# Optimization experiments

Hardware: AMD Instinct MI355X
Metric: run time of the kernel (lower is better)

## Reference

```python
import jax, jax.numpy as jnp
import numpy as np

L, N, D, T = 24, 576, 4096, 128
RED = D // 4           # DSU reduced dim (reduction_ratio=4)
FOCUS = (-2) % L       # focus layer index = 22
EPS_LN = 1e-5          # torch LayerNorm default eps
EPS_SC = 1e-6          # score-normalization eps
N_FOCUS = 32           # final_focus (hardcoded in forward)
N_NONFOCUS = 32        # final_nonfocus (hardcoded in forward)
MIN_ACTIVE = 8
THRESH = 3.0


def _ln(x, g=None, b=None):
    mu = x.mean(-1, keepdims=True)
    var = ((x - mu) ** 2).mean(-1, keepdims=True)
    y = (x - mu) / jnp.sqrt(var + EPS_LN)
    if g is not None:
        y = y * g + b
    return y


def setup_inputs() -> dict:
    key = jax.random.key(0)
    ks = jax.random.split(key, 10)
    rn = lambda k, shape, s=0.02: jax.random.normal(k, shape, jnp.float32) * s
    z = lambda n: jnp.zeros((n,), jnp.float32)
    return {
        'text_features': jax.random.normal(ks[0], (T, D), jnp.float32),
        'layer_feats': jax.random.normal(ks[1], (L, N, D), jnp.float32),
        'W1': rn(ks[2], (RED, 3 * D)), 'b1': z(RED),
        'Wc': rn(ks[3], (D, RED)), 'bc_lin': z(D), 'bc': z(D),
        'Wi': rn(ks[4], (D, RED)), 'bi_lin': z(D), 'bi': z(D),
        'Wf': rn(ks[5], (D, RED)), 'bf_lin': z(D), 'bf': z(D),
        'score_q_w': rn(ks[6], (D, D)), 'score_k_w': rn(ks[7], (D, D)),
        'ln_g': jnp.ones((D,), jnp.float32), 'ln_b': z(D),
        'layer_logits': rn(ks[8], (L,), 0.1),
        'scale': jnp.array([0.1], jnp.float32),
    }


def reference(text_features, layer_feats, W1, b1, Wc, bc_lin, bc, Wi, bi_lin, bi,
              Wf, bf_lin, bf, score_q_w, score_k_w, ln_g, ln_b, layer_logits, scale):
    # --- text conditioning ---
    text_global = _ln(text_features.mean(0))                 # [D]
    y = layer_feats.mean(1)                                   # [L, D] per-layer pooled

    # --- DSU recurrence over layers (LSTM-like cell) ---
    def dsu(c_prev, y_l):
        comb = jnp.concatenate([jax.nn.sigmoid(c_prev), y_l, text_global])
        s = jax.nn.relu(W1 @ comb + b1)                       # [RED]
        c_t = jnp.tanh(Wc @ s + bc_lin + bc)
        i = jax.nn.sigmoid(Wi @ s + bi_lin + bi)
        f = jax.nn.sigmoid(Wf @ s + bf_lin + bf)
        c = f * c_prev + i * c_t
        return c, c

    _, ctx = jax.lax.scan(dsu, jnp.zeros((D,), text_features.dtype), y)  # [L, D]

    # --- per-layer scores with LayerNorm'd q/k ---
    q = _ln(ctx @ score_q_w.T, ln_g, ln_b)                    # [L, D]
    kf = _ln(layer_feats @ score_k_w.T, ln_g, ln_b)           # [L, N, D]
    raw = jnp.einsum('lnd,ld->ln', kf, q)                     # [L, N]
    mu = raw.mean(1, keepdims=True)
    sd = raw.std(1, keepdims=True) + EPS_SC                   # unbiased=False
    scores = (raw - mu) / sd                                  # [L, N]
    conf = scores.max(1)                                      # [L]

    # --- active-layer selection (threshold path vs top-8 fallback) ---
    nonfocus = jnp.ones((L,), bool).at[FOCUS].set(False)
    conf_nf = jnp.where(nonfocus, conf, -jnp.inf)
    act_t = nonfocus & (conf > THRESH)
    M_t = act_t.sum()
    _, idx_f = jax.lax.top_k(conf_nf, MIN_ACTIVE)             # fallback: top-8 conf, desc
    act_f = jnp.zeros((L,), bool).at[idx_f].set(True)
    pos_f = jnp.full((L,), L, jnp.int32).at[idx_f].set(jnp.arange(MIN_ACTIVE, dtype=jnp.int32))
    pos_t = jnp.cumsum(act_t.astype(jnp.int32)) - 1           # ascending layer order
    use_fb = M_t < MIN_ACTIVE
    act = jnp.where(use_fb, act_f, act_t)
    pos = jnp.where(use_fb, pos_f, pos_t)
    M = jnp.where(use_fb, MIN_ACTIVE, M_t)

    # --- budget split: base per active layer + remainder to earliest (N=576 >> 32, no deficit) ---
    base = N_NONFOCUS // M
    rem = N_NONFOCUS - base * M
    k_nf = jnp.where(act, base + (pos < rem).astype(jnp.int32), 0)  # [L], sums to 32

    # --- per-layer top-32 indices (sorted desc), gather evidence ---
    _, top_idx = jax.lax.top_k(scores, N_FOCUS)               # [L, 32]
    ev_focus = layer_feats[FOCUS][top_idx[FOCUS]]             # [32, D]
    cum = jnp.cumsum(k_nf)                                    # [L]
    t = jnp.arange(N_NONFOCUS)
    li = jnp.searchsorted(cum, t, side='right')               # owning layer per slot
    r = t - (cum[li] - k_nf[li])                              # rank within layer
    ev_nf = layer_feats[li, top_idx[li, r]]                   # [32, D]

    # --- anchor-residual layer mix + 3x3 group pooling ---
    logits = layer_logits.astype(jnp.float32).at[FOCUS].set(-jnp.inf)
    alpha = jax.nn.softmax(logits)                            # [L], alpha[anchor]=0
    anchor = layer_feats[FOCUS]                               # [N, D]
    delta = jnp.einsum('l,lnd->nd', alpha, layer_feats - anchor[None])
    x_mix = anchor + scale[0] * delta                         # [576, D]
    groups = x_mix.reshape(3, 8, 3, 8, D).transpose(0, 2, 1, 3, 4).reshape(9, 64, D).mean(1)

    return jnp.concatenate([ev_focus, ev_nf, groups], 0)      # [73, D]
```

## Files before the change

### kernel.cpp

```cpp
#include <hip/hip_runtime.h>
#include <stdint.h>
#include <math.h>

#define LAY 24
#define NTOK 576
#define DIM 4096
#define TTXT 128
#define REDD 1024
#define FOCUSL 22

typedef unsigned int u32;
typedef unsigned short u16;
typedef float f32x4 __attribute__((ext_vector_type(4)));
typedef short bf16x8 __attribute__((ext_vector_type(8)));
typedef u16 u16x4 __attribute__((ext_vector_type(4)));

__device__ __forceinline__ u16 f2bf(float f) {
  u32 u = __builtin_bit_cast(u32, f);
  u32 r = u + 0x7fffu + ((u >> 16) & 1u);
  return (u16)(r >> 16);
}
__device__ __forceinline__ float sigm(float x) { return 1.0f / (1.0f + expf(-x)); }

#define GLOBAL_AS __attribute__((address_space(1)))
#define LDS_AS __attribute__((address_space(3)))
__device__ __forceinline__ void gld_lds16(const void* g, void* l) {
  __builtin_amdgcn_global_load_lds((const GLOBAL_AS u32*)g, (LDS_AS u32*)l, 16, 0, 0);
}

__global__ void k_text_colmean(const float* __restrict__ tf, float* __restrict__ tmean) {
  int c = blockIdx.x * 256 + threadIdx.x;
  float s = 0.f;
  for (int r = 0; r < TTXT; r++) s += tf[(size_t)r * DIM + c];
  tmean[c] = s * (1.0f / TTXT);
}

__global__ void k_text_ln(const float* __restrict__ tmean, float* __restrict__ tg) {
  __shared__ float red[256];
  int t = threadIdx.x;
  float x[16]; float s = 0.f;
  for (int i = 0; i < 16; i++) { x[i] = tmean[i * 256 + t]; s += x[i]; }
  red[t] = s; __syncthreads();
  for (int o = 128; o; o >>= 1) { if (t < o) red[t] += red[t + o]; __syncthreads(); }
  float mean = red[0] / DIM; __syncthreads();
  float q = 0.f;
  for (int i = 0; i < 16; i++) { float d = x[i] - mean; q += d * d; }
  red[t] = q; __syncthreads();
  for (int o = 128; o; o >>= 1) { if (t < o) red[t] += red[t + o]; __syncthreads(); }
  float var = red[0] / DIM;
  float rinv = 1.0f / sqrtf(var + 1e-5f);
  for (int i = 0; i < 16; i++) tg[i * 256 + t] = (x[i] - mean) * rinv;
}

__global__ void k_pass_a(const float* __restrict__ x, u16* __restrict__ xb,
                         float* __restrict__ gm) {
  int bid = blockIdx.x;
  int a = bid % 3, dc = (bid / 3) & 7, l = bid / 24;
  int d4 = dc * 512 + threadIdx.x * 4;
  f32x4 acc[3] = {};
  int n0 = a * 192;
  const float* p = x + ((size_t)(l * NTOK + n0)) * DIM + d4;
  u16* q = xb + ((size_t)(l * NTOK + n0)) * DIM + d4;
  for (int nn = 0; nn < 192; nn++) {
    f32x4 v = *(const f32x4*)p;
    u16x4 bv; bv.x = f2bf(v.x); bv.y = f2bf(v.y); bv.z = f2bf(v.z); bv.w = f2bf(v.w);
    *(u16x4*)q = bv;
    int c = (nn >> 3) % 3;
    acc[c] += v;
    p += DIM; q += DIM;
  }
  for (int c = 0; c < 3; c++) {
    f32x4 o = acc[c] * (1.0f / 64.0f);
    *(f32x4*)(gm + ((size_t)(l * 9 + a * 3 + c)) * DIM + d4) = o;
  }
}

__global__ void k_y(const float* __restrict__ gm, float* __restrict__ y) {
  int bid = blockIdx.x;
  int l = bid >> 2, dc = bid & 3;
  int d4 = dc * 1024 + threadIdx.x * 4;
  f32x4 s = {};
  for (int g = 0; g < 9; g++) s += *(const f32x4*)(gm + ((size_t)(l * 9 + g)) * DIM + d4);
  *(f32x4*)(y + (size_t)l * DIM + d4) = s * (1.0f / 9.0f);
}

__global__ void k_conv_wk(const float* __restrict__ wk, u16* __restrict__ wkb) {
  size_t i = (size_t)blockIdx.x * 256 + threadIdx.x;
  f32x4 v = ((const f32x4*)wk)[i];
  u16x4 b; b.x = f2bf(v.x); b.y = f2bf(v.y); b.z = f2bf(v.z); b.w = f2bf(v.w);
  ((u16x4*)wkb)[i] = b;
}

__global__ __launch_bounds__(256) void k_gemm_s2(const u16* __restrict__ xb,
                                                 const u16* __restrict__ wkb,
                                                 float* __restrict__ s2p) {
  __shared__ __align__(16) u16 As[128 * 32];
  __shared__ __align__(16) u16 Bs[128 * 32];
  int bid = blockIdx.x;
  int mt = bid >> 5, nt = bid & 31;
  int tid = threadIdx.x;
  int wid = tid >> 6, lane = tid & 63;
  int wm = (wid >> 1) * 64, wn = (wid & 1) * 64;
  int lm = lane & 15, qq = lane >> 4;
  f32x4 acc[4][4] = {};
  const u16* gA = xb + (size_t)(mt * 128) * DIM;
  const u16* gB = wkb + (size_t)(nt * 128) * DIM;
  for (int kt = 0; kt < DIM / 32; kt++) {
    int k0 = kt * 32;
    __syncthreads();
    for (int j = 0; j < 2; j++) {
      int seg = tid + 256 * j;
      int row = seg >> 2, ko = (seg & 3) * 8;
      gld_lds16(gA + (size_t)row * DIM + k0 + ko, &As[seg * 8]);
      gld_lds16(gB + (size_t)row * DIM + k0 + ko, &Bs[seg * 8]);
    }
    __syncthreads();
    bf16x8 aF[4], bF[4];
    for (int mi = 0; mi < 4; mi++) aF[mi] = *(const bf16x8*)&As[(wm + mi * 16 + lm) * 32 + qq * 8];
    for (int ni = 0; ni < 4; ni++) bF[ni] = *(const bf16x8*)&Bs[(wn + ni * 16 + lm) * 32 + qq * 8];
    for (int mi = 0; mi < 4; mi++)
      for (int ni = 0; ni < 4; ni++)
        acc[mi][ni] = __builtin_amdgcn_mfma_f32_16x16x32_bf16(aF[mi], bF[ni], acc[mi][ni], 0, 0, 0);
  }
  for (int mi = 0; mi < 4; mi++) {
    for (int reg = 0; reg < 4; reg++) {
      float s = 0.f;
      for (int ni = 0; ni < 4; ni++) { float v = acc[mi][ni][reg]; s += v * v; }
      for (int off = 1; off < 16; off <<= 1) s += __shfl_xor(s, off, 64);
      if (lm == 0) {
        int row = mt * 128 + wm + mi * 16 + qq * 4 + reg;
        s2p[(size_t)row * 64 + nt * 2 + (wid & 1)] = s;
      }
    }
  }
}

__global__ void k_s2_reduce(const float* __restrict__ s2p, float* __restrict__ S2) {
  int row = blockIdx.x * 256 + threadIdx.x;
  const f32x4* p = (const f32x4*)(s2p + (size_t)row * 64);
  float s = 0.f;
  for (int i = 0; i < 16; i++) { f32x4 v = p[i]; s += v.x + v.y + v.z + v.w; }
  S2[row] = s;
}

__global__ __launch_bounds__(256) void k_pre(const float* __restrict__ W1, const float* __restrict__ b1,
                                             const float* __restrict__ y, const float* __restrict__ tg,
                                             float* __restrict__ pre) {
  int r = blockIdx.x, t = threadIdx.x;
  __shared__ float ylds[LAY][256];
  __shared__ float tglds[256];
  __shared__ float red[256];
  float acc[LAY]; for (int l = 0; l < LAY; l++) acc[l] = 0.f;
  float accc = 0.f;
  const float* wb = W1 + (size_t)r * (3 * DIM) + DIM;
  const float* wc = W1 + (size_t)r * (3 * DIM) + 2 * DIM;
  for (int ch = 0; ch < 16; ch++) {
    for (int l = 0; l < LAY; l++) ylds[l][t] = y[(size_t)l * DIM + ch * 256 + t];
    tglds[t] = tg[ch * 256 + t];
    __syncthreads();
    float w1b = wb[ch * 256 + t];
    float w1c = wc[ch * 256 + t];
    for (int l = 0; l < LAY; l++) acc[l] += w1b * ylds[l][t];
    accc += w1c * tglds[t];
    __syncthreads();
  }
  red[t] = accc; __syncthreads();
  for (int o = 128; o; o >>= 1) { if (t < o) red[t] += red[t + o]; __syncthreads(); }
  float csum = red[0]; __syncthreads();
  for (int l = 0; l < LAY; l++) {
    red[t] = acc[l]; __syncthreads();
    for (int o = 128; o; o >>= 1) { if (t < o) red[t] += red[t + o]; __syncthreads(); }
    if (t == 0) pre[l * REDD + r] = b1[r] + red[0] + csum;
    __syncthreads();
  }
}

__global__ void k_dsu_init(float* __restrict__ c_prev, float* __restrict__ u) {
  int i = blockIdx.x * 256 + threadIdx.x;
  c_prev[i] = 0.0f;
  u[i] = 0.5f;
}

__global__ __launch_bounds__(256) void k_dsu1(const float* __restrict__ W1, const float* __restrict__ pre,
                                              const float* __restrict__ u, float* __restrict__ svec,
                                              int l) {
  __shared__ __align__(16) float ulds[DIM];
  int b = blockIdx.x, t = threadIdx.x;
  int wid = t >> 6, lane = t & 63;
  for (int i = 0; i < 16; i++) ulds[i * 256 + t] = u[i * 256 + t];
  __syncthreads();
  int r = b * 4 + wid;
  const float* wrow = W1 + (size_t)r * (3 * DIM);
  float acc = 0.f;
  for (int i = 0; i < 16; i++) {
    int e = i * 256 + lane * 4;
    f32x4 w = *(const f32x4*)(wrow + e);
    f32x4 uv = *(const f32x4*)(&ulds[e]);
    acc += w.x * uv.x + w.y * uv.y + w.z * uv.z + w.w * uv.w;
  }
  for (int off = 32; off; off >>= 1) acc += __shfl_down(acc, off, 64);
  if (lane == 0) {
    float sv = acc + pre[l * REDD + r];
    svec[r] = sv > 0.f ? sv : 0.f;
  }
}

__global__ __launch_bounds__(256) void k_dsu2(
    const float* __restrict__ Wc, const float* __restrict__ Wi, const float* __restrict__ Wf,
    const float* __restrict__ bc_lin, const float* __restrict__ bc,
    const float* __restrict__ bi_lin, const float* __restrict__ bi,
    const float* __restrict__ bf_lin, const float* __restrict__ bf,
    const float* __restrict__ svec, float* __restrict__ c_prev, float* __restrict__ u,
    float* __restrict__ ctx, int l) {
  __shared__ __align__(16) float sl[REDD];
  int b = blockIdx.x, t = threadIdx.x;
  int wid = t >> 6, lane = t & 63;
  for (int i = 0; i < 4; i++) sl[i * 256 + t] = svec[i * 256 + t];
  __syncthreads();
  int d = b * 4 + wid;
  float g3[3];
  for (int gate = 0; gate < 3; gate++) {
    const float* wrow = (gate == 0 ? Wc : (gate == 1 ? Wi : Wf)) + (size_t)d * REDD;
    float acc = 0.f;
    for (int i = 0; i < 4; i++) {
      int k = i * 256 + lane * 4;
      f32x4 w = *(const f32x4*)(wrow + k);
      f32x4 sv = *(const f32x4*)(&sl[k]);
      acc += w.x * sv.x + w.y * sv.y + w.z * sv.z + w.w * sv.w;
    }
    for (int off = 32; off; off >>= 1) acc += __shfl_down(acc, off, 64);
    g3[gate] = acc;
  }
  if (lane == 0) {
    float ct = tanhf(g3[0] + bc_lin[d] + bc[d]);
    float iv = sigm(g3[1] + bi_lin[d] + bi[d]);
    float fv = sigm(g3[2] + bf_lin[d] + bf[d]);
    float c = fv * c_prev[d] + iv * ct;
    c_prev[d] = c;
    u[d] = sigm(c);
    ctx[(size_t)l * DIM + d] = c;
  }
}

__global__ __launch_bounds__(256) void k_qpre(const float* __restrict__ ctx, const float* __restrict__ Wq,
                                              float* __restrict__ qpre) {
  __shared__ __align__(16) float clds[LAY][512];
  int b = blockIdx.x, t = threadIdx.x;
  int wid = t >> 6, lane = t & 63;
  int e = b * 4 + wid;
  const float* wrow = Wq + (size_t)e * DIM;
  float acc[LAY]; for (int l = 0; l < LAY; l++) acc[l] = 0.f;
  for (int ch = 0; ch < 8; ch++) {
    for (int i = 0; i < 48; i++) {
      int idx = i * 256 + t;
      int l = idx >> 9, dd = idx & 511;
      clds[l][dd] = ctx[(size_t)l * DIM + ch * 512 + dd];
    }
    __syncthreads();
    for (int i = 0; i < 2; i++) {
      int dd = i * 256 + lane * 4;
      f32x4 w = *(const f32x4*)(wrow + ch * 512 + dd);
      for (int l = 0; l < LAY; l++) {
        f32x4 c = *(const f32x4*)(&clds[l][dd]);
        acc[l] += w.x * c.x + w.y * c.y + w.z * c.z + w.w * c.w;
      }
    }
    __syncthreads();
  }
  for (int l = 0; l < LAY; l++) {
    float s = acc[l];
    for (int off = 32; off; off >>= 1) s += __shfl_down(s, off, 64);
    if (lane == 0) qpre[(size_t)l * DIM + e] = s;
  }
}

__global__ void k_qln(const float* __restrict__ qpre, const float* __restrict__ g, const float* __restrict__ bb,
                      float* __restrict__ h, float* __restrict__ A, float* __restrict__ Bv) {
  int l = blockIdx.x, t = threadIdx.x;
  __shared__ float red[256];
  float x[16]; float s = 0.f;
  for (int i = 0; i < 16; i++) { x[i] = qpre[(size_t)l * DIM + i * 256 + t]; s += x[i]; }
  red[t] = s; __syncthreads();
  for (int o = 128; o; o >>= 1) { if (t < o) red[t] += red[t + o]; __syncthreads(); }
  float mean = red[0] / DIM; __syncthreads();
  float qs = 0.f;
  for (int i = 0; i < 16; i++) { float dd = x[i] - mean; qs += dd * dd; }
  red[t] = qs; __syncthreads();
  for (int o = 128; o; o >>= 1) { if (t < o) red[t] += red[t + o]; __syncthreads(); }
  float var = red[0] / DIM;
  float rinv = 1.0f / sqrtf(var + 1e-5f);
  float sa = 0.f, sb = 0.f;
  for (int i = 0; i < 16; i++) {
    int d = i * 256 + t;
    float gv = g[d], bv = bb[d];
    float qv = (x[i] - mean) * rinv * gv + bv;
    float hv = gv * qv;
    h[(size_t)l * DIM + d] = hv;
    sa += hv; sb += bv * qv;
  }
  __syncthreads();
  red[t] = sa; __syncthreads();
  for (int o = 128; o; o >>= 1) { if (t < o) red[t] += red[t + o]; __syncthreads(); }
  if (t == 0) A[l] = red[0];
  __syncthreads();
  red[t] = sb; __syncthreads();
  for (int o = 128; o; o >>= 1) { if (t < o) red[t] += red[t + o]; __syncthreads(); }
  if (t == 0) Bv[l] = red[0];
}

__global__ __launch_bounds__(256) void k_v(const float* __restrict__ Wk, const float* __restrict__ h,
                                           float* __restrict__ v, float* __restrict__ wmu) {
  int eb = blockIdx.x & 15, db = blockIdx.x >> 4;
  int t = threadIdx.x;
  __shared__ float hl[LAY][256];
  for (int l = 0; l < LAY; l++) hl[l][t] = h[(size_t)l * DIM + db * 256 + t];
  __syncthreads();
  int e = eb * 256 + t;
  float acc[LAY]; for (int l = 0; l < LAY; l++) acc[l] = 0.f;
  float am = 0.f;
  for (int dd = 0; dd < 256; dd++) {
    float w = Wk[(size_t)(db * 256 + dd) * DIM + e];
    am += w;
    for (int l = 0; l < LAY; l++) acc[l] += w * hl[l][dd];
  }
  for (int l = 0; l < LAY; l++) atomicAdd(&v[(size_t)l * DIM + e], acc[l]);
  atomicAdd(&wmu[e], am * (1.0f / DIM));
}

__global__ __launch_bounds__(256) void k_dotmu(const float* __restrict__ x, const float* __restrict__ v,
                                               const float* __restrict__ wmu, float* __restrict__ dotv,
                                               float* __restrict__ muv) {
  __shared__ __align__(16) float vl[DIM];
  __shared__ __align__(16) float wm[DIM];
  int bid = blockIdx.x;
  int l = bid / 144, n4 = bid % 144;
  int t = threadIdx.x, wid = t >> 6, lane = t & 63;
  for (int i = 0; i < 16; i++) {
    int idx = i * 256 + t;
    vl[idx] = v[(size_t)l * DIM + idx];
    wm[idx] = wmu[idx];
  }
  __syncthreads();
  int n = n4 * 4 + wid;
  const float* row = x + (size_t)(l * NTOK + n) * DIM;
  float ad = 0.f, am = 0.f;
  for (int i = 0; i < 16; i++) {
    int e = i * 256 + lane * 4;
    f32x4 xv = *(const f32x4*)(row + e);
    f32x4 vv = *(const f32x4*)(&vl[e]);
    f32x4 wv = *(const f32x4*)(&wm[e]);
    ad += xv.x * vv.x + xv.y * vv.y + xv.z * vv.z + xv.w * vv.w;
    am += xv.x * wv.x + xv.y * wv.y + xv.z * wv.z + xv.w * wv.w;
  }
  for (int off = 32; off; off >>= 1) { ad += __shfl_down(ad, off, 64); am += __shfl_down(am, off, 64); }
  if (lane == 0) { dotv[l * NTOK + n] = ad; muv[l * NTOK + n] = am; }
}

__global__ void k_scores(const float* __restrict__ dotv, const float* __restrict__ muv,
                         const float* __restrict__ S2, const float* __restrict__ A, const float* __restrict__ Bv,
                         int* __restrict__ topidx, float* __restrict__ conf) {
  int l = blockIdx.x, t = threadIdx.x;
  __shared__ float raw[NTOK];
  __shared__ float rv[256];
  __shared__ float wv4[4]; __shared__ int wi4[4];
  int wid = t >> 6, lane = t & 63;
  float Al = A[l], Bl = Bv[l];
  for (int j = t; j < NTOK; j += 256) {
    float dv = dotv[l * NTOK + j], mv = muv[l * NTOK + j];
    float var = S2[l * NTOK + j] * (1.0f / DIM) - mv * mv;
    float sd = sqrtf(var + 1e-5f);
    raw[j] = (dv - mv * Al) / sd + Bl;
  }
  __syncthreads();
  float s = 0.f;
  for (int j = t; j < NTOK; j += 256) s += raw[j];
  rv[t] = s; __syncthreads();
  for (int o = 128; o; o >>= 1) { if (t < o) rv[t] += rv[t + o]; __syncthreads(); }
  float mean = rv[0] / NTOK; __syncthreads();
  float qsum = 0.f;
  for (int j = t; j < NTOK; j += 256) { float d = raw[j] - mean; qsum += d * d; }
  rv[t] = qsum; __syncthreads();
  for (int o = 128; o; o >>= 1) { if (t < o) rv[t] += rv[t + o]; __syncthreads(); }
  float sdn = sqrtf(rv[0] / NTOK) + 1e-6f; __syncthreads();
  for (int k = 0; k < 32; k++) {
    float bv = -INFINITY; int bi = NTOK;
    for (int j = t; j < NTOK; j += 256) {
      float vv = raw[j];
      if (vv > bv || (vv == bv && j < bi)) { bv = vv; bi = j; }
    }
    for (int off = 32; off; off >>= 1) {
      float ov = __shfl_down(bv, off, 64); int oi = __shfl_down(bi, off, 64);
      if (ov > bv || (ov == bv && oi < bi)) { bv = ov; bi = oi; }
    }
    if (lane == 0) { wv4[wid] = bv; wi4[wid] = bi; }
    __syncthreads();
    if (t == 0) {
      float b2 = wv4[0]; int i2 = wi4[0];
      for (int w2 = 1; w2 < 4; w2++)
        if (wv4[w2] > b2 || (wv4[w2] == b2 && wi4[w2] < i2)) { b2 = wv4[w2]; i2 = wi4[w2]; }
      topidx[l * 32 + k] = i2;
      if (k == 0) conf[l] = (b2 - mean) / sdn;
      raw[i2] = -INFINITY;
    }
    __syncthreads();
  }
}

__global__ void k_select(const float* __restrict__ conf, const int* __restrict__ topidx,
                         const float* __restrict__ logits,
                         int* __restrict__ src, float* __restrict__ alpha) {
  if (threadIdx.x != 0 || blockIdx.x != 0) return;
  float cf[LAY]; for (int l = 0; l < LAY; l++) cf[l] = conf[l];
  bool actt[LAY]; int Mt = 0;
  for (int l = 0; l < LAY; l++) { actt[l] = (l != FOCUSL) && (cf[l] > 3.0f); if (actt[l]) Mt++; }
  bool act[LAY]; int pos[LAY]; int M;
  if (Mt < 8) {
    float cnf[LAY];
    for (int l = 0; l < LAY; l++) cnf[l] = (l == FOCUSL) ? -INFINITY : cf[l];
    bool used[LAY] = {};
    for (int l = 0; l < LAY; l++) { act[l] = false; pos[l] = LAY; }
    for (int j = 0; j < 8; j++) {
      float bv = -INFINITY; int bidx = -1;
      for (int l = 0; l < LAY; l++) if (!used[l] && cnf[l] > bv) { bv = cnf[l]; bidx = l; }
      used[bidx] = true; act[bidx] = true; pos[bidx] = j;
    }
    M = 8;
  } else {
    int c = 0;
    for (int l = 0; l < LAY; l++) { act[l] = actt[l]; if (actt[l]) { pos[l] = c; c++; } else pos[l] = -1; }
    M = Mt;
  }
  int base = 32 / M, rem = 32 - base * M;
  int kk[LAY]; int cum[LAY]; int run = 0;
  for (int l = 0; l < LAY; l++) {
    int k = act[l] ? (base + ((pos[l] < rem) ? 1 : 0)) : 0;
    kk[l] = k; run += k; cum[l] = run;
  }
  for (int tt = 0; tt < 32; tt++) src[tt] = FOCUSL * NTOK + topidx[FOCUSL * 32 + tt];
  for (int tt = 0; tt < 32; tt++) {
    int li = 0;
    while (cum[li] <= tt) li++;
    int r = tt - (cum[li] - kk[li]);
    src[32 + tt] = li * NTOK + topidx[li * 32 + r];
  }
  float mx = -INFINITY;
  for (int l = 0; l < LAY; l++) if (l != FOCUSL && logits[l] > mx) mx = logits[l];
  float ssum = 0.f; float av[LAY];
  for (int l = 0; l < LAY; l++) { av[l] = (l == FOCUSL) ? 0.0f : expf(logits[l] - mx); ssum += av[l]; }
  for (int l = 0; l < LAY; l++) alpha[l] = av[l] / ssum;
}

__global__ void k_gather(const float* __restrict__ x, const int* __restrict__ src, float* __restrict__ out) {
  int b = blockIdx.x, t = threadIdx.x;
  const float* row = x + (size_t)src[b] * DIM;
  float* o = out + (size_t)b * DIM;
  for (int i = 0; i < 4; i++) {
    int e = (i * 256 + t) * 4;
    *(f32x4*)(o + e) = *(const f32x4*)(row + e);
  }
}

__global__ void k_groups(const float* __restrict__ gm, const float* __restrict__ alpha,
                         const float* __restrict__ scale, float* __restrict__ out) {
  int g = blockIdx.x, t = threadIdx.x;
  float sc = scale[0];
  __shared__ float al[LAY];
  if (t < LAY) al[t] = alpha[t];
  __syncthreads();
  for (int i = 0; i < 4; i++) {
    int d = (i * 256 + t) * 4;
    f32x4 mix = {};
    for (int l = 0; l < LAY; l++) {
      f32x4 gv = *(const f32x4*)(gm + ((size_t)(l * 9 + g)) * DIM + d);
      mix += gv * al[l];
    }
    f32x4 anc = *(const f32x4*)(gm + ((size_t)(FOCUSL * 9 + g)) * DIM + d);
    f32x4 o = anc + (mix - anc) * sc;
    *(f32x4*)(out + (size_t)(64 + g) * DIM + d) = o;
  }
}

extern "C" void kernel_launch(void* const* d_in, const int* in_sizes, int n_in,
                              void* d_out, int out_size, void* d_ws, size_t ws_size,
                              hipStream_t stream) {
  const float* tf     = (const float*)d_in[0];
  const float* x      = (const float*)d_in[1];
  const float* W1     = (const float*)d_in[2];
  const float* b1     = (const float*)d_in[3];
  const float* Wc     = (const float*)d_in[4];
  const float* bc_lin = (const float*)d_in[5];
  const float* bc     = (const float*)d_in[6];
  const float* Wi     = (const float*)d_in[7];
  const float* bi_lin = (const float*)d_in[8];
  const float* bi     = (const float*)d_in[9];
  const float* Wf     = (const float*)d_in[10];
  const float* bf_lin = (const float*)d_in[11];
  const float* bf     = (const float*)d_in[12];
  const float* Wq     = (const float*)d_in[13];
  const float* Wk     = (const float*)d_in[14];
  const float* ln_g   = (const float*)d_in[15];
  const float* ln_b   = (const float*)d_in[16];
  const float* logits = (const float*)d_in[17];
  const float* scale  = (const float*)d_in[18];
  float* out = (float*)d_out;

  char* w = (char*)d_ws;
  size_t off = 0;
  auto alloc = [&](size_t bytes) -> void* {
    void* p = w + off;
    off += (bytes + 255) & ~(size_t)255;
    return p;
  };
  float* v    = (float*)alloc((size_t)LAY * DIM * 4);
  float* wmu  = (float*)alloc((size_t)DIM * 4);
  size_t zero_bytes = off;
  u16* xb     = (u16*)alloc((size_t)LAY * NTOK * DIM * 2);
  u16* wkb    = (u16*)alloc((size_t)DIM * DIM * 2);
  float* gm   = (float*)alloc((size_t)LAY * 9 * DIM * 4);
  float* y    = (float*)alloc((size_t)LAY * DIM * 4);
  float* tmean= (float*)alloc((size_t)DIM * 4);
  float* tg   = (float*)alloc((size_t)DIM * 4);
  float* pre  = (float*)alloc((size_t)LAY * REDD * 4);
  float* svec = (float*)alloc((size_t)REDD * 4);
  float* cprev= (float*)alloc((size_t)DIM * 4);
  float* uvec = (float*)alloc((size_t)DIM * 4);
  float* ctx  = (float*)alloc((size_t)LAY * DIM * 4);
  float* qpre = (float*)alloc((size_t)LAY * DIM * 4);
  float* h    = (float*)alloc((size_t)LAY * DIM * 4);
  float* A    = (float*)alloc((size_t)LAY * 4);
  float* Bv   = (float*)alloc((size_t)LAY * 4);
  float* s2p  = (float*)alloc((size_t)LAY * NTOK * 64 * 4);
  float* S2   = (float*)alloc((size_t)LAY * NTOK * 4);
  float* dotv = (float*)alloc((size_t)LAY * NTOK * 4);
  float* muv  = (float*)alloc((size_t)LAY * NTOK * 4);
  int* topidx = (int*)alloc((size_t)LAY * 32 * 4);
  float* conf = (float*)alloc((size_t)LAY * 4);
  int* src    = (int*)alloc(64 * 4);
  float* alph = (float*)alloc((size_t)LAY * 4);
  (void)in_sizes; (void)n_in; (void)out_size; (void)ws_size;

  hipMemsetAsync(d_ws, 0, zero_bytes, stream);
  k_text_colmean<<<16, 256, 0, stream>>>(tf, tmean);
  k_text_ln<<<1, 256, 0, stream>>>(tmean, tg);
  k_pass_a<<<576, 128, 0, stream>>>(x, xb, gm);
  k_y<<<96, 256, 0, stream>>>(gm, y);
  k_conv_wk<<<16384, 256, 0, stream>>>(Wk, wkb);
  k_gemm_s2<<<108 * 32, 256, 0, stream>>>(xb, wkb, s2p);
  k_s2_reduce<<<54, 256, 0, stream>>>(s2p, S2);
  k_pre<<<1024, 256, 0, stream>>>(W1, b1, y, tg, pre);
  k_dsu_init<<<16, 256, 0, stream>>>(cprev, uvec);
  for (int l = 0; l < LAY; l++) {
    k_dsu1<<<256, 256, 0, stream>>>(W1, pre, uvec, svec, l);
    k_dsu2<<<1024, 256, 0, stream>>>(Wc, Wi, Wf, bc_lin, bc, bi_lin, bi, bf_lin, bf,
                                     svec, cprev, uvec, ctx, l);
  }
  k_qpre<<<1024, 256, 0, stream>>>(ctx, Wq, qpre);
  k_qln<<<24, 256, 0, stream>>>(qpre, ln_g, ln_b, h, A, Bv);
  k_v<<<256, 256, 0, stream>>>(Wk, h, v, wmu);
  k_dotmu<<<24 * 144, 256, 0, stream>>>(x, v, wmu, dotv, muv);
  k_scores<<<24, 256, 0, stream>>>(dotv, muv, S2, A, Bv, topidx, conf);
  k_select<<<1, 64, 0, stream>>>(conf, topidx, logits, src, alph);
  k_gather<<<64, 256, 0, stream>>>(x, src, out);
  k_groups<<<9, 256, 0, stream>>>(gm, alph, scale, out);
}
```

Before: 2.055 ms.

## Fuse DSU recurrence into one cooperative kernel and swizzle GEMM LDS layout

Replaces the 49 per-layer DSU kernel launches with a single cooperative kernel of 256 blocks that uses grid-wide syncs between the W1 matvec and gate phases, so per-launch overhead goes away. Each block now handles 16 output dims in the gate phase instead of 4. Separately, the s2 GEMM now XOR-swizzles k-chunks in LDS to reduce bank conflicts on fragment reads. In exchange, grid.sync costs are added and the DSU runs on fewer blocks, so each block carries more memory traffic.

```diff
diff --git a/kernel.cpp b/kernel.cpp
--- a/kernel.cpp
+++ b/kernel.cpp
@@ -1,6 +1,9 @@
 #include <hip/hip_runtime.h>
+#include <hip/hip_cooperative_groups.h>
 #include <stdint.h>
 #include <math.h>
+
+namespace cg = cooperative_groups;
 
 #define LAY 24
 #define NTOK 576
@@ -105,19 +108,29 @@
   f32x4 acc[4][4] = {};
   const u16* gA = xb + (size_t)(mt * 128) * DIM;
   const u16* gB = wkb + (size_t)(nt * 128) * DIM;
+  int aslot[4], bslot[4];
+  for (int mi = 0; mi < 4; mi++) {
+    int R = wm + mi * 16 + lm;
+    aslot[mi] = R * 4 + (qq ^ ((R >> 1) & 3));
+  }
+  for (int ni = 0; ni < 4; ni++) {
+    int R = wn + ni * 16 + lm;
+    bslot[ni] = R * 4 + (qq ^ ((R >> 1) & 3));
+  }
   for (int kt = 0; kt < DIM / 32; kt++) {
     int k0 = kt * 32;
     __syncthreads();
     for (int j = 0; j < 2; j++) {
       int seg = tid + 256 * j;
-      int row = seg >> 2, ko = (seg & 3) * 8;
-      gld_lds16(gA + (size_t)row * DIM + k0 + ko, &As[seg * 8]);
-      gld_lds16(gB + (size_t)row * DIM + k0 + ko, &Bs[seg * 8]);
+      int row = seg >> 2;
+      int kc = (seg & 3) ^ ((row >> 1) & 3);
+      gld_lds16(gA + (size_t)row * DIM + k0 + kc * 8, &As[seg * 8]);
+      gld_lds16(gB + (size_t)row * DIM + k0 + kc * 8, &Bs[seg * 8]);
     }
     __syncthreads();
     bf16x8 aF[4], bF[4];
-    for (int mi = 0; mi < 4; mi++) aF[mi] = *(const bf16x8*)&As[(wm + mi * 16 + lm) * 32 + qq * 8];
-    for (int ni = 0; ni < 4; ni++) bF[ni] = *(const bf16x8*)&Bs[(wn + ni * 16 + lm) * 32 + qq * 8];
+    for (int mi = 0; mi < 4; mi++) aF[mi] = *(const bf16x8*)&As[aslot[mi] * 8];
+    for (int ni = 0; ni < 4; ni++) bF[ni] = *(const bf16x8*)&Bs[bslot[ni] * 8];
     for (int mi = 0; mi < 4; mi++)
       for (int ni = 0; ni < 4; ni++)
         acc[mi][ni] = __builtin_amdgcn_mfma_f32_16x16x32_bf16(aF[mi], bF[ni], acc[mi][ni], 0, 0, 0);
@@ -175,70 +188,69 @@
   }
 }
 
-__global__ void k_dsu_init(float* __restrict__ c_prev, float* __restrict__ u) {
-  int i = blockIdx.x * 256 + threadIdx.x;
-  c_prev[i] = 0.0f;
-  u[i] = 0.5f;
-}
-
-__global__ __launch_bounds__(256) void k_dsu1(const float* __restrict__ W1, const float* __restrict__ pre,
-                                              const float* __restrict__ u, float* __restrict__ svec,
-                                              int l) {
-  __shared__ __align__(16) float ulds[DIM];
-  int b = blockIdx.x, t = threadIdx.x;
-  int wid = t >> 6, lane = t & 63;
-  for (int i = 0; i < 16; i++) ulds[i * 256 + t] = u[i * 256 + t];
-  __syncthreads();
-  int r = b * 4 + wid;
-  const float* wrow = W1 + (size_t)r * (3 * DIM);
-  float acc = 0.f;
-  for (int i = 0; i < 16; i++) {
-    int e = i * 256 + lane * 4;
-    f32x4 w = *(const f32x4*)(wrow + e);
-    f32x4 uv = *(const f32x4*)(&ulds[e]);
-    acc += w.x * uv.x + w.y * uv.y + w.z * uv.z + w.w * uv.w;
-  }
-  for (int off = 32; off; off >>= 1) acc += __shfl_down(acc, off, 64);
-  if (lane == 0) {
-    float sv = acc + pre[l * REDD + r];
-    svec[r] = sv > 0.f ? sv : 0.f;
-  }
-}
-
-__global__ __launch_bounds__(256) void k_dsu2(
+__global__ __launch_bounds__(256, 1) void k_dsu_coop(
+    const float* __restrict__ W1, const float* __restrict__ pre,
     const float* __restrict__ Wc, const float* __restrict__ Wi, const float* __restrict__ Wf,
     const float* __restrict__ bc_lin, const float* __restrict__ bc,
     const float* __restrict__ bi_lin, const float* __restrict__ bi,
     const float* __restrict__ bf_lin, const float* __restrict__ bf,
-    const float* __restrict__ svec, float* __restrict__ c_prev, float* __restrict__ u,
-    float* __restrict__ ctx, int l) {
-  __shared__ __align__(16) float sl[REDD];
+    float* __restrict__ c_prev, float* __restrict__ u,
+    float* __restrict__ svec, float* __restrict__ ctx) {
+  cg::grid_group grid = cg::this_grid();
+  __shared__ __align__(16) float ulds[DIM];
+  __shared__ __align__(16) float slds[REDD];
   int b = blockIdx.x, t = threadIdx.x;
   int wid = t >> 6, lane = t & 63;
-  for (int i = 0; i < 4; i++) sl[i * 256 + t] = svec[i * 256 + t];
-  __syncthreads();
-  int d = b * 4 + wid;
-  float g3[3];
-  for (int gate = 0; gate < 3; gate++) {
-    const float* wrow = (gate == 0 ? Wc : (gate == 1 ? Wi : Wf)) + (size_t)d * REDD;
-    float acc = 0.f;
-    for (int i = 0; i < 4; i++) {
-      int k = i * 256 + lane * 4;
-      f32x4 w = *(const f32x4*)(wrow + k);
-      f32x4 sv = *(const f32x4*)(&sl[k]);
-      acc += w.x * sv.x + w.y * sv.y + w.z * sv.z + w.w * sv.w;
-    }
-    for (int off = 32; off; off >>= 1) acc += __shfl_down(acc, off, 64);
-    g3[gate] = acc;
-  }
-  if (lane == 0) {
-    float ct = tanhf(g3[0] + bc_lin[d] + bc[d]);
-    float iv = sigm(g3[1] + bi_lin[d] + bi[d]);
-    float fv = sigm(g3[2] + bf_lin[d] + bf[d]);
-    float c = fv * c_prev[d] + iv * ct;
-    c_prev[d] = c;
-    u[d] = sigm(c);
-    ctx[(size_t)l * DIM + d] = c;
+  if (t < 16) { c_prev[b * 16 + t] = 0.0f; u[b * 16 + t] = 0.5f; }
+  grid.sync();
+  for (int l = 0; l < LAY; l++) {
+    for (int i = 0; i < 16; i++) ulds[i * 256 + t] = u[i * 256 + t];
+    __syncthreads();
+    {
+      int r = b * 4 + wid;
+      const float* wrow = W1 + (size_t)r * (3 * DIM);
+      float acc = 0.f;
+      for (int i = 0; i < 16; i++) {
+        int e = i * 256 + lane * 4;
+        f32x4 w = *(const f32x4*)(wrow + e);
+        f32x4 uv = *(const f32x4*)(&ulds[e]);
+        acc += w.x * uv.x + w.y * uv.y + w.z * uv.z + w.w * uv.w;
+      }
+      for (int off = 32; off; off >>= 1) acc += __shfl_down(acc, off, 64);
+      if (lane == 0) {
+        float sv = acc + pre[l * REDD + r];
+        svec[r] = sv > 0.f ? sv : 0.f;
+      }
+    }
+    grid.sync();
+    for (int i = 0; i < 4; i++) slds[i * 256 + t] = svec[i * 256 + t];
+    __syncthreads();
+    for (int j = 0; j < 4; j++) {
+      int d = b * 16 + wid * 4 + j;
+      float g3[3];
+      for (int gate = 0; gate < 3; gate++) {
+        const float* wrow = (gate == 0 ? Wc : (gate == 1 ? Wi : Wf)) + (size_t)d * REDD;
+        float acc = 0.f;
+        for (int i = 0; i < 4; i++) {
+          int k = i * 256 + lane * 4;
+          f32x4 w = *(const f32x4*)(wrow + k);
+          f32x4 sv = *(const f32x4*)(&slds[k]);
+          acc += w.x * sv.x + w.y * sv.y + w.z * sv.z + w.w * sv.w;
+        }
+        for (int off = 32; off; off >>= 1) acc += __shfl_down(acc, off, 64);
+        g3[gate] = acc;
+      }
+      if (lane == 0) {
+        float ct = tanhf(g3[0] + bc_lin[d] + bc[d]);
+        float iv = sigm(g3[1] + bi_lin[d] + bi[d]);
+        float fv = sigm(g3[2] + bf_lin[d] + bf[d]);
+        float c = fv * c_prev[d] + iv * ct;
+        c_prev[d] = c;
+        u[d] = sigm(c);
+        ctx[(size_t)l * DIM + d] = c;
+      }
+    }
+    grid.sync();
   }
 }
 
@@ -548,11 +560,12 @@
   k_gemm_s2<<<108 * 32, 256, 0, stream>>>(xb, wkb, s2p);
   k_s2_reduce<<<54, 256, 0, stream>>>(s2p, S2);
   k_pre<<<1024, 256, 0, stream>>>(W1, b1, y, tg, pre);
-  k_dsu_init<<<16, 256, 0, stream>>>(cprev, uvec);
-  for (int l = 0; l < LAY; l++) {
-    k_dsu1<<<256, 256, 0, stream>>>(W1, pre, uvec, svec, l);
-    k_dsu2<<<1024, 256, 0, stream>>>(Wc, Wi, Wf, bc_lin, bc, bi_lin, bi, bf_lin, bf,
-                                     svec, cprev, uvec, ctx, l);
+  {
+    void* args[] = {(void*)&W1, (void*)&pre, (void*)&Wc, (void*)&Wi, (void*)&Wf,
+                    (void*)&bc_lin, (void*)&bc, (void*)&bi_lin, (void*)&bi,
+                    (void*)&bf_lin, (void*)&bf, (void*)&cprev, (void*)&uvec,
+                    (void*)&svec, (void*)&ctx};
+    hipLaunchCooperativeKernel((const void*)k_dsu_coop, dim3(256), dim3(256), args, 0, stream);
   }
   k_qpre<<<1024, 256, 0, stream>>>(ctx, Wq, qpre);
   k_qln<<<24, 256, 0, stream>>>(qpre, ln_g, ln_b, h, A, Bv);
```

Result: slower. 3.327 ms (+61.9%).
